# Kernel tuning notes

Hardware: AMD Instinct MI355X
Metric: run time of the kernel (lower is better)

## Reference

```python
import jax, jax.numpy as jnp
import numpy as np

C_M, C_Z, C = 256, 128, 32
N_SEQ, N_RES = 128, 256


def setup_inputs() -> dict:
    key = jax.random.key(0)
    ks = jax.random.split(key, 9)
    s = 0.02
    return {
        "m": jax.random.normal(ks[0], (N_SEQ, N_RES, C_M), dtype=jnp.float32),
        "ln_w": jnp.ones((C_M,), dtype=jnp.float32),
        "ln_b": jnp.zeros((C_M,), dtype=jnp.float32),
        "w1": jax.random.normal(ks[1], (C, C_M), dtype=jnp.float32) * s,
        "b1": jnp.zeros((C,), dtype=jnp.float32),
        "w2": jax.random.normal(ks[2], (C, C_M), dtype=jnp.float32) * s,
        "b2": jnp.zeros((C,), dtype=jnp.float32),
        "wo": jax.random.normal(ks[3], (C_Z, C * C), dtype=jnp.float32) * s,
        "bo": jnp.zeros((C_Z,), dtype=jnp.float32),
    }


def reference(m, ln_w, ln_b, w1, b1, w2, b2, wo, bo):
    n_seq = m.shape[-3]
    # LayerNorm over c_m
    mu = jnp.mean(m, axis=-1, keepdims=True)
    var = jnp.mean(jnp.square(m - mu), axis=-1, keepdims=True)
    mn = (m - mu) * jax.lax.rsqrt(var + 1e-5) * ln_w + ln_b
    # dual projections to c channels: [s, i, c]
    a = jnp.einsum('sim,cm->sic', mn, w1) + b1
    b = jnp.einsum('sjm,dm->sjd', mn, w2) + b2
    # outer product mean contracted over sequence axis: [i, j, c, d]
    o = jnp.einsum('sic,sjd->ijcd', a, b)
    o = o.reshape(o.shape[0], o.shape[1], C * C)
    # output projection and mean over sequences
    z = (jnp.einsum('ijk,zk->ijz', o, wo) + bo) / n_seq
    return z
```

## Files before the change

### kernel.cpp

```cpp
#include <hip/hip_runtime.h>
#include <hip/hip_bf16.h>
#include <stdint.h>

#define N_RES 256
#define CMDIM 256

typedef __attribute__((ext_vector_type(8))) short bf16x8;
typedef __attribute__((ext_vector_type(4))) float f32x4;
typedef __attribute__((ext_vector_type(2))) unsigned int u32x2;

__device__ __forceinline__ unsigned short f32_to_bf16(float f) {
    union { float f; unsigned int u; } v; v.f = f;
    unsigned int u = v.u;
    return (unsigned short)((u + 0x7FFFu + ((u >> 16) & 1u)) >> 16);
}

__device__ __forceinline__ int swz5(int x) {
    return ((x >> 2) & 7) | (((x >> 5) & 1) << 3) | ((x & 1) << 4);
}


__global__ __launch_bounds__(256) void k_ln_proj(
    const float* __restrict__ m, const float* __restrict__ lnw, const float* __restrict__ lnb,
    const float* __restrict__ w1, const float* __restrict__ b1,
    const float* __restrict__ w2, const float* __restrict__ b2,
    const float* __restrict__ wo,
    unsigned short* __restrict__ A2f, unsigned short* __restrict__ B2f,
    unsigned short* __restrict__ wof)
{
    __shared__ unsigned short mn[32 * 256];
    __shared__ unsigned short stg[2048];
    int b = blockIdx.x;
    int i = b >> 2, sblk = b & 3;
    int tid = threadIdx.x;
    int wv = tid >> 6, lane = tid & 63;
    int quad = lane >> 4, l15 = lane & 15;

    if (tid < 128) {
        int t = b * 128 + tid;
        int zo = t >> 10, k = t & 1023;
        int addr = ((zo >> 4) * 32 + (k >> 5)) * 512 + ((k >> 3) & 3) * 128 + (zo & 15) * 8 + (k & 7);
        wof[addr] = f32_to_bf16(wo[t]);
    }

    f32x4 lw = *(const f32x4*)(lnw + lane * 4);
    f32x4 lb = *(const f32x4*)(lnb + lane * 4);

    #pragma unroll
    for (int r = 0; r < 8; ++r) {
        int sl = wv * 8 + r;
        int s = sblk * 32 + sl;
        const float* row = m + ((size_t)s * N_RES + i) * CMDIM;
        f32x4 x = *(const f32x4*)(row + lane * 4);
        float s1 = x[0] + x[1] + x[2] + x[3];
        float s2 = x[0]*x[0] + x[1]*x[1] + x[2]*x[2] + x[3]*x[3];
        #pragma unroll
        for (int off = 32; off; off >>= 1) {
            s1 += __shfl_xor(s1, off);
            s2 += __shfl_xor(s2, off);
        }
        float mu = s1 * (1.0f / 256.0f);
        float var = s2 * (1.0f / 256.0f) - mu * mu;
        float rstd = rsqrtf(var + 1e-5f);
        float n0 = (x[0] - mu) * rstd * lw[0] + lb[0];
        float n1 = (x[1] - mu) * rstd * lw[1] + lb[1];
        float n2 = (x[2] - mu) * rstd * lw[2] + lb[2];
        float n3 = (x[3] - mu) * rstd * lw[3] + lb[3];
        unsigned int p0 = (unsigned)f32_to_bf16(n0) | ((unsigned)f32_to_bf16(n1) << 16);
        unsigned int p1 = (unsigned)f32_to_bf16(n2) | ((unsigned)f32_to_bf16(n3) << 16);
        int chunk = lane >> 1;
        int pos = (chunk & 16) | ((chunk ^ sl) & 15);
        unsigned int* dst = (unsigned int*)((char*)mn + sl * 512 + pos * 16 + (lane & 1) * 8);
        dst[0] = p0; dst[1] = p1;
    }

    const float* wrow = (wv < 2) ? (w1 + (size_t)(wv * 16 + l15) * 256)
                                 : (w2 + (size_t)((wv - 2) * 16 + l15) * 256);
    bf16x8 af[8];
    #pragma unroll
    for (int ks = 0; ks < 8; ++ks) {
        f32x4 lo = *(const f32x4*)(wrow + ks * 32 + quad * 8);
        f32x4 hi = *(const f32x4*)(wrow + ks * 32 + quad * 8 + 4);
        bf16x8 f;
        f[0] = (short)f32_to_bf16(lo[0]);
        f[1] = (short)f32_to_bf16(lo[1]);
        f[2] = (short)f32_to_bf16(lo[2]);
        f[3] = (short)f32_to_bf16(lo[3]);
        f[4] = (short)f32_to_bf16(hi[0]);
        f[5] = (short)f32_to_bf16(hi[1]);
        f[6] = (short)f32_to_bf16(hi[2]);
        f[7] = (short)f32_to_bf16(hi[3]);
        af[ks] = f;
    }

    __syncthreads();

    f32x4 acc[2];
    acc[0] = (f32x4){0.f, 0.f, 0.f, 0.f};
    acc[1] = (f32x4){0.f, 0.f, 0.f, 0.f};
    #pragma unroll
    for (int ks = 0; ks < 8; ++ks) {
        #pragma unroll
        for (int nb = 0; nb < 2; ++nb) {
            int sl = nb * 16 + l15;
            int chunk = ks * 4 + quad;
            int pos = (chunk & 16) | ((chunk ^ sl) & 15);
            bf16x8 bf = *(const bf16x8*)((char*)mn + sl * 512 + pos * 16);
            acc[nb] = __builtin_amdgcn_mfma_f32_16x16x32_bf16(af[ks], bf, acc[nb], 0, 0, 0);
        }
    }

    const float* bsrc = (wv < 2) ? b1 : b2;
    f32x4 bias = *(const f32x4*)(bsrc + (wv & 1) * 16 + quad * 4);
    unsigned short* sbase = stg + (wv >> 1) * 1024 + (wv & 1) * 512 + quad * 32;
    #pragma unroll
    for (int nb = 0; nb < 2; ++nb) {
        int sl = nb * 16 + l15;
        int soff = ((sl >> 3) & 3) * 128 + (sl & 7);
        #pragma unroll
        for (int reg = 0; reg < 4; ++reg)
            sbase[soff + reg * 8] = f32_to_bf16(acc[nb][reg] + bias[reg]);
    }
    __syncthreads();

    int part = tid >> 7, blk = (tid >> 6) & 1, l = tid & 63;
    unsigned short* gdst = (part ? B2f : A2f) + ((i * 2 + blk) * 4 + sblk) * 512 + l * 8;
    *(bf16x8*)gdst = *(const bf16x8*)(stg + tid * 8);
}

__global__ __launch_bounds__(512, 2) void k_fused(
    const unsigned short* __restrict__ A2f, const unsigned short* __restrict__ B2f,
    const unsigned short* __restrict__ wof, const float* __restrict__ bo,
    float* __restrict__ out)
{
    __shared__ char olds[65536];
    int bid = blockIdx.x;
    int sb = (bid & 7) * 256 + (bid >> 3);
    int bx = sb & 63, by = sb >> 6;
    int tid = threadIdx.x, wv = tid >> 6, lane = tid & 63;
    int quad = lane >> 4, l15 = lane & 15;
    int pass = wv >> 2, wm = (wv >> 1) & 1, wn = wv & 1;

    const unsigned short* Abase = A2f + (size_t)((bx * 8 + wn * 4) * 4) * 512 + lane * 8;
    const unsigned short* Bbase = B2f + (size_t)((by * 16 + pass * 8 + wm * 4) * 4) * 512 + lane * 8;

    bf16x8 bn[4][4], am[4][4];
    #pragma unroll
    for (int nb = 0; nb < 4; ++nb)
        #pragma unroll
        for (int ks = 0; ks < 4; ++ks)
            bn[ks][nb] = *(const bf16x8*)(Abase + (size_t)(nb * 4 + ks) * 512);
    #pragma unroll
    for (int mb = 0; mb < 4; ++mb)
        #pragma unroll
        for (int ks = 0; ks < 4; ++ks)
            am[ks][mb] = *(const bf16x8*)(Bbase + (size_t)(mb * 4 + ks) * 512);

    f32x4 acc[4][4];
    #pragma unroll
    for (int a = 0; a < 4; ++a)
        #pragma unroll
        for (int b = 0; b < 4; ++b) acc[a][b] = (f32x4){0.f, 0.f, 0.f, 0.f};

    __builtin_amdgcn_s_setprio(1);
    #pragma unroll
    for (int ks = 0; ks < 4; ++ks)
        #pragma unroll
        for (int mb = 0; mb < 4; ++mb)
            #pragma unroll
            for (int nb = 0; nb < 4; ++nb)
                acc[mb][nb] = __builtin_amdgcn_mfma_f32_16x16x32_bf16(am[ks][mb], bn[ks][nb], acc[mb][nb], 0, 0, 0);
    __builtin_amdgcn_s_setprio(0);

    #pragma unroll
    for (int mb = 0; mb < 4; ++mb) {
        int m_ = wm * 64 + mb * 16 + quad * 4;
        int d0 = m_ & 31;
        int jl = pass * 4 + (m_ >> 5);
        #pragma unroll
        for (int nb = 0; nb < 4; ++nb) {
            int n_ = wn * 64 + nb * 16 + l15;
            int c = n_ & 31, il = n_ >> 5;
            int pair = il * 8 + jl;
            int e0 = c * 32 + d0;
            int chunk = e0 >> 3;
            int phys = pair ^ swz5(chunk);
            f32x4 a4 = acc[mb][nb];
            unsigned int p0 = (unsigned)f32_to_bf16(a4[0]) | ((unsigned)f32_to_bf16(a4[1]) << 16);
            unsigned int p1 = (unsigned)f32_to_bf16(a4[2]) | ((unsigned)f32_to_bf16(a4[3]) << 16);
            u32x2 pv = {p0, p1};
            *(u32x2*)(olds + chunk * 512 + phys * 16 + (e0 & 7) * 2) = pv;
        }
    }

    int zg = wv >> 1, kh = wv & 1, kt0 = kh * 16;
    const unsigned short* wbase = wof + lane * 8;
    bf16x8 wreg[2][16];
    #pragma unroll
    for (int zb = 0; zb < 2; ++zb)
        #pragma unroll
        for (int kt = 0; kt < 16; ++kt)
            wreg[zb][kt] = *(const bf16x8*)(wbase + (size_t)(((2 * zg + zb) * 32) + kt0 + kt) * 512);

    __syncthreads();

    f32x4 acc2[2][2];
    #pragma unroll
    for (int a = 0; a < 2; ++a)
        #pragma unroll
        for (int b = 0; b < 2; ++b) acc2[a][b] = (f32x4){0.f, 0.f, 0.f, 0.f};

    #pragma unroll
    for (int kt = 0; kt < 16; ++kt) {
        bf16x8 bfr[2];
        #pragma unroll
        for (int pb = 0; pb < 2; ++pb) {
            int pair = pb * 16 + l15;
            int chunk = (kt0 + kt) * 4 + quad;
            int phys = pair ^ swz5(chunk);
            bfr[pb] = *(const bf16x8*)(olds + chunk * 512 + phys * 16);
        }
        #pragma unroll
        for (int zb = 0; zb < 2; ++zb)
            #pragma unroll
            for (int pb = 0; pb < 2; ++pb)
                acc2[zb][pb] = __builtin_amdgcn_mfma_f32_16x16x32_bf16(
                    wreg[zb][kt], bfr[pb], acc2[zb][pb], 0, 0, 0);
    }

    __syncthreads();
    f32x4* red = (f32x4*)olds;
    if (kh == 1) {
        #pragma unroll
        for (int zb = 0; zb < 2; ++zb)
            #pragma unroll
            for (int pb = 0; pb < 2; ++pb)
                red[(((zg * 2 + zb) * 2 + pb) << 6) + quad * 16 + l15] = acc2[zb][pb];
    }
    __syncthreads();
    if (kh == 0) {
        #pragma unroll
        for (int zb = 0; zb < 2; ++zb) {
            int zo = zg * 32 + zb * 16 + quad * 4;
            f32x4 b4 = *(const f32x4*)(bo + zo);
            #pragma unroll
            for (int pb = 0; pb < 2; ++pb) {
                f32x4 part = red[(((zg * 2 + zb) * 2 + pb) << 6) + quad * 16 + l15];
                int pair = pb * 16 + l15;
                int i = bx * 4 + (pair >> 3);
                int j = by * 8 + (pair & 7);
                f32x4 v;
                #pragma unroll
                for (int reg = 0; reg < 4; ++reg)
                    v[reg] = (acc2[zb][pb][reg] + part[reg] + b4[reg]) * (1.0f / 128.0f);
                *(f32x4*)(out + ((size_t)(i * 256 + j)) * 128 + zo) = v;
            }
        }
    }
}

extern "C" void kernel_launch(void* const* d_in, const int* in_sizes, int n_in,
                              void* d_out, int out_size, void* d_ws, size_t ws_size,
                              hipStream_t stream) {
    const float* m   = (const float*)d_in[0];
    const float* lnw = (const float*)d_in[1];
    const float* lnb = (const float*)d_in[2];
    const float* w1  = (const float*)d_in[3];
    const float* b1  = (const float*)d_in[4];
    const float* w2  = (const float*)d_in[5];
    const float* b2  = (const float*)d_in[6];
    const float* wo  = (const float*)d_in[7];
    const float* bo  = (const float*)d_in[8];
    float* out = (float*)d_out;
    char* ws = (char*)d_ws;

    unsigned short* wof = (unsigned short*)(ws + 32768);
    unsigned short* A2f = (unsigned short*)(ws + 32768 + 262144);
    unsigned short* B2f = (unsigned short*)(ws + 32768 + 262144 + 2097152);

    hipLaunchKernelGGL(k_ln_proj, dim3(1024), dim3(256), 0, stream,
                       m, lnw, lnb, w1, b1, w2, b2, wo, A2f, B2f, wof);
    hipLaunchKernelGGL(k_fused, dim3(2048), dim3(512), 0, stream,
                       A2f, B2f, wof, bo, out);
}
```

Measured before the change: 153.7 us.

## Stream output-projection weights through LDS with async global_load_lds pipeline

```diff
diff --git a/kernel.cpp b/kernel.cpp
--- a/kernel.cpp
+++ b/kernel.cpp
@@ -8,6 +8,10 @@
 typedef __attribute__((ext_vector_type(8))) short bf16x8;
 typedef __attribute__((ext_vector_type(4))) float f32x4;
 typedef __attribute__((ext_vector_type(2))) unsigned int u32x2;
+
+typedef const __attribute__((address_space(1))) void* gas1_t;
+typedef __attribute__((address_space(3))) void* las3_t;
+#define GLDS(g, l) __builtin_amdgcn_global_load_lds((gas1_t)(g), (las3_t)(l), 16, 0, 0)
 
 __device__ __forceinline__ unsigned short f32_to_bf16(float f) {
     union { float f; unsigned int u; } v; v.f = f;
@@ -128,18 +132,29 @@
     *(bf16x8*)gdst = *(const bf16x8*)(stg + tid * 8);
 }
 
-__global__ __launch_bounds__(512, 2) void k_fused(
+__global__ __launch_bounds__(512, 1) void k_fused(
     const unsigned short* __restrict__ A2f, const unsigned short* __restrict__ B2f,
     const unsigned short* __restrict__ wof, const float* __restrict__ bo,
     float* __restrict__ out)
 {
     __shared__ char olds[65536];
+    __shared__ char wofbuf[65536];
     int bid = blockIdx.x;
     int sb = (bid & 7) * 256 + (bid >> 3);
     int bx = sb & 63, by = sb >> 6;
     int tid = threadIdx.x, wv = tid >> 6, lane = tid & 63;
     int quad = lane >> 4, l15 = lane & 15;
     int pass = wv >> 2, wm = (wv >> 1) & 1, wn = wv & 1;
+
+    int zg = wv >> 1, kh = wv & 1, kt0 = kh * 16;
+    char* wslab = wofbuf + wv * 8192;
+    const unsigned short* wsrc0 = wof + (size_t)((2 * zg) * 32 + kt0) * 512 + lane * 8;
+    const unsigned short* wsrc1 = wof + (size_t)((2 * zg + 1) * 32 + kt0) * 512 + lane * 8;
+    #pragma unroll
+    for (int c = 0; c < 3; ++c) {
+        GLDS(wsrc0 + (size_t)c * 512, wslab + c * 2048);
+        GLDS(wsrc1 + (size_t)c * 512, wslab + c * 2048 + 1024);
+    }
 
     const unsigned short* Abase = A2f + (size_t)((bx * 8 + wn * 4) * 4) * 512 + lane * 8;
     const unsigned short* Bbase = B2f + (size_t)((by * 16 + pass * 8 + wm * 4) * 4) * 512 + lane * 8;
@@ -193,15 +208,6 @@
         }
     }
 
-    int zg = wv >> 1, kh = wv & 1, kt0 = kh * 16;
-    const unsigned short* wbase = wof + lane * 8;
-    bf16x8 wreg[2][16];
-    #pragma unroll
-    for (int zb = 0; zb < 2; ++zb)
-        #pragma unroll
-        for (int kt = 0; kt < 16; ++kt)
-            wreg[zb][kt] = *(const bf16x8*)(wbase + (size_t)(((2 * zg + zb) * 32) + kt0 + kt) * 512);
-
     __syncthreads();
 
     f32x4 acc2[2][2];
@@ -212,20 +218,29 @@
 
     #pragma unroll
     for (int kt = 0; kt < 16; ++kt) {
-        bf16x8 bfr[2];
-        #pragma unroll
-        for (int pb = 0; pb < 2; ++pb) {
-            int pair = pb * 16 + l15;
-            int chunk = (kt0 + kt) * 4 + quad;
-            int phys = pair ^ swz5(chunk);
-            bfr[pb] = *(const bf16x8*)(olds + chunk * 512 + phys * 16);
-        }
-        #pragma unroll
-        for (int zb = 0; zb < 2; ++zb)
-            #pragma unroll
-            for (int pb = 0; pb < 2; ++pb)
-                acc2[zb][pb] = __builtin_amdgcn_mfma_f32_16x16x32_bf16(
-                    wreg[zb][kt], bfr[pb], acc2[zb][pb], 0, 0, 0);
+        if (kt == 15)      asm volatile("s_waitcnt vmcnt(0)" ::: "memory");
+        else if (kt == 14) asm volatile("s_waitcnt vmcnt(2)" ::: "memory");
+        else               asm volatile("s_waitcnt vmcnt(4)" ::: "memory");
+
+        const char* slab = wslab + (kt & 3) * 2048;
+        bf16x8 af0 = *(const bf16x8*)(slab + lane * 16);
+        bf16x8 af1 = *(const bf16x8*)(slab + 1024 + lane * 16);
+        int chunk = (kt0 + kt) * 4 + quad;
+        int sz = swz5(chunk);
+        bf16x8 bfr0 = *(const bf16x8*)(olds + chunk * 512 + (l15 ^ sz) * 16);
+        bf16x8 bfr1 = *(const bf16x8*)(olds + chunk * 512 + ((16 + l15) ^ sz) * 16);
+
+        __builtin_amdgcn_s_setprio(1);
+        acc2[0][0] = __builtin_amdgcn_mfma_f32_16x16x32_bf16(af0, bfr0, acc2[0][0], 0, 0, 0);
+        acc2[0][1] = __builtin_amdgcn_mfma_f32_16x16x32_bf16(af0, bfr1, acc2[0][1], 0, 0, 0);
+        acc2[1][0] = __builtin_amdgcn_mfma_f32_16x16x32_bf16(af1, bfr0, acc2[1][0], 0, 0, 0);
+        acc2[1][1] = __builtin_amdgcn_mfma_f32_16x16x32_bf16(af1, bfr1, acc2[1][1], 0, 0, 0);
+        __builtin_amdgcn_s_setprio(0);
+
+        if (kt + 3 < 16) {
+            GLDS(wsrc0 + (size_t)(kt + 3) * 512, wslab + ((kt + 3) & 3) * 2048);
+            GLDS(wsrc1 + (size_t)(kt + 3) * 512, wslab + ((kt + 3) & 3) * 2048 + 1024);
+        }
     }
 
     __syncthreads();
```

Result: slower. 157.1 us (+2.2%).
